# Optimization experiments

Hardware: AMD Instinct MI355X
Metric: run time of the kernel (lower is better)

The kernel has to match this reference:

```python
import jax, jax.numpy as jnp
import numpy as np

G = 56          # voxel grid resolution per axis
N = 65536
K = 27          # 3x3x3 kernel offsets
C_IN = 128
C_OUT = 128


def _build_rulebook():
    """Submanifold conv rulebook: for each kernel offset, (input_row, output_row) pairs.

    Padded to P=N pairs per offset; invalid pairs use in_idx=0 and out_idx=N
    (a dummy output slot that is dropped), so shapes are static.
    """
    rng = np.random.default_rng(0)
    keys = np.sort(rng.choice(G ** 3, size=N, replace=False)).astype(np.int64)
    x = keys // (G * G)
    y = (keys // G) % G
    z = keys % G
    in_idx = np.zeros((K, N), dtype=np.int32)
    out_idx = np.full((K, N), N, dtype=np.int32)
    k = 0
    for dx in (-1, 0, 1):
        for dy in (-1, 0, 1):
            for dz in (-1, 0, 1):
                nx, ny, nz = x + dx, y + dy, z + dz
                valid = (nx >= 0) & (nx < G) & (ny >= 0) & (ny < G) & (nz >= 0) & (nz < G)
                nkey = (nx * G + ny) * G + nz
                pos = np.searchsorted(keys, np.clip(nkey, 0, G ** 3 - 1))
                pos = np.clip(pos, 0, N - 1)
                found = valid & (keys[pos] == nkey)
                cnt = int(found.sum())
                in_idx[k, :cnt] = pos[found]
                out_idx[k, :cnt] = np.nonzero(found)[0]
                k += 1
    return jnp.asarray(in_idx), jnp.asarray(out_idx)


def setup_inputs() -> dict:
    key = jax.random.key(0)
    k1, k2, k3 = jax.random.split(key, 3)
    fan_in = K * C_IN
    features = jax.random.normal(k1, (N, C_IN), dtype=jnp.float32)
    weight = jax.random.normal(k2, (K, C_IN, C_OUT), dtype=jnp.float32) * (1.0 / np.sqrt(fan_in))
    bias = jax.random.normal(k3, (C_OUT,), dtype=jnp.float32) * 0.01
    in_idx, out_idx = _build_rulebook()
    return {"features": features, "weight": weight, "bias": bias,
            "in_idx": in_idx, "out_idx": out_idx}


def reference(features, weight, bias, in_idx, out_idx):
    # gather: [K, P, C_in]
    gathered = features[in_idx]
    # per-offset GEMM: [K, P, C_out]
    contrib = jnp.einsum('kpc,kcd->kpd', gathered, weight)
    n = features.shape[0]
    c_out = weight.shape[-1]
    # scatter-accumulate into N real rows + 1 dummy row for padded pairs
    out = jnp.zeros((n + 1, c_out), dtype=features.dtype)
    out = out.at[out_idx.reshape(-1)].add(contrib.reshape(-1, c_out))
    return out[:n] + bias
```

## Files before the change

### kernel.cpp

```cpp
#include <hip/hip_runtime.h>
#include <hip/hip_bf16.h>
#include <stdint.h>

#define NV   65536
#define KOFF 27
#define CIN  128
#define COUT 128

typedef __bf16 bf16x8 __attribute__((ext_vector_type(8)));
typedef float  f32x16 __attribute__((ext_vector_type(16)));

__device__ __forceinline__ void async_copy16(void* lds, const void* g) {
    __builtin_amdgcn_global_load_lds(
        (const __attribute__((address_space(1))) void*)g,
        (__attribute__((address_space(3))) void*)lds,
        16, 0, 0);
}

#define JOB_A_BLOCKS 4097
#define JOB_B_BLOCKS 108
#define JOB_S_BLOCKS 1728

__global__ void k_prep_all(const float* __restrict__ f,
                           uint4* __restrict__ fb4,
                           const float* __restrict__ w,
                           __hip_bfloat16* __restrict__ wt,
                           const int4* __restrict__ in4,
                           const int4* __restrict__ out4,
                           int* __restrict__ nbr) {
    __shared__ float tb[64][65];
    const int b = blockIdx.x;
    const int t = threadIdx.x;
    if (b < JOB_A_BLOCKS) {
        int i = b * 256 + t;
        int total8  = (NV + 1) * CIN / 8;
        int nvalid8 = NV * CIN / 8;
        if (i >= total8) return;
        union { uint4 u; __hip_bfloat16 h[8]; } p;
        if (i < nvalid8) {
            const float4* f4 = (const float4*)f;
            float4 a = f4[i * 2];
            float4 c = f4[i * 2 + 1];
            p.h[0] = __float2bfloat16(a.x);
            p.h[1] = __float2bfloat16(a.y);
            p.h[2] = __float2bfloat16(a.z);
            p.h[3] = __float2bfloat16(a.w);
            p.h[4] = __float2bfloat16(c.x);
            p.h[5] = __float2bfloat16(c.y);
            p.h[6] = __float2bfloat16(c.z);
            p.h[7] = __float2bfloat16(c.w);
        } else {
            p.u = make_uint4(0, 0, 0, 0);
        }
        fb4[i] = p.u;
    } else if (b < JOB_A_BLOCKS + JOB_B_BLOCKS) {
        int bb = b - JOB_A_BLOCKS;
        int k    = bb >> 2;
        int r0   = ((bb >> 1) & 1) * 64;
        int c0   = (bb & 1) * 64;
        const float* wk = w + k * 16384;
        __hip_bfloat16* wtk = wt + k * 16384;
        #pragma unroll
        for (int j = 0; j < 16; ++j) {
            int lrow = j * 4 + (t >> 6);
            int lcol = t & 63;
            tb[lrow][lcol] = wk[(r0 + lrow) * 128 + (c0 + lcol)];
        }
        __syncthreads();
        #pragma unroll
        for (int j = 0; j < 16; ++j) {
            int orow = j * 4 + (t >> 6);
            int ocol = t & 63;
            wtk[(c0 + orow) * 128 + (r0 + ocol)] = __float2bfloat16(tb[ocol][orow]);
        }
    } else {
        int i = (b - JOB_A_BLOCKS - JOB_B_BLOCKS) * 256 + t;
        int k = i >> 14;
        int4 ii = in4[i];
        int4 oo = out4[i];
        int* nb = nbr + k * (NV + 1);
        nb[oo.x] = ii.x;
        nb[oo.y] = ii.y;
        nb[oo.z] = ii.z;
        nb[oo.w] = ii.w;
    }
}

__global__ __launch_bounds__(256, 2)
void sp_conv_main(const __hip_bfloat16* __restrict__ feats,
                  const __hip_bfloat16* __restrict__ wt,
                  const int* __restrict__ nbr,
                  const float* __restrict__ bias,
                  float* __restrict__ out) {
    __shared__ unsigned char smem[65536];
    unsigned char* smA = smem;
    unsigned char* smB = smem + 32768;

    const int t   = threadIdx.x;
    const int bid = blockIdx.x;
    const int tile0 = ((bid & 7) * 64 + (bid >> 3)) * 128;

    const int w    = t >> 6;
    const int lane = t & 63;
    const int l31  = lane & 31;
    const int half = lane >> 5;
    const int m0   = (w >> 1) * 64;
    const int n0   = (w & 1) * 64;

    const int srow   = t >> 4;
    const int sbyte  = ((t & 15) ^ srow) * 16;

    f32x16 acc[2][2] = {};

    const unsigned char* featsB = (const unsigned char*)feats;
    const unsigned char* wtB    = (const unsigned char*)wt;

    int arows[8];
    {
        const int* nbr0 = nbr + tile0;
        #pragma unroll
        for (int i = 0; i < 8; ++i) arows[i] = nbr0[i * 16 + srow];
    }

    for (int k = 0; k < KOFF; ++k) {
        const unsigned char* wk = wtB + (size_t)k * 32768;
        #pragma unroll
        for (int i = 0; i < 8; ++i) {
            unsigned ar = min((unsigned)arows[i], (unsigned)NV);
            async_copy16(smA + i * 4096 + t * 16,
                         featsB + (size_t)ar * 256 + sbyte);
            async_copy16(smB + i * 4096 + t * 16,
                         wk + (i * 16 + srow) * 256 + sbyte);
        }
        __syncthreads();

        if (k + 1 < KOFF) {
            const int* nbrn = nbr + (k + 1) * (NV + 1) + tile0;
            #pragma unroll
            for (int i = 0; i < 8; ++i) arows[i] = nbrn[i * 16 + srow];
        }

        #pragma unroll
        for (int ks = 0; ks < 8; ++ks) {
            const int c = ks * 2 + half;
            bf16x8 af[2], bfr[2];
            #pragma unroll
            for (int mt = 0; mt < 2; ++mt) {
                int row = m0 + mt * 32 + l31;
                af[mt] = *(const bf16x8*)(smA + row * 256 + ((c ^ (row & 15)) * 16));
            }
            #pragma unroll
            for (int nt = 0; nt < 2; ++nt) {
                int row = n0 + nt * 32 + l31;
                bfr[nt] = *(const bf16x8*)(smB + row * 256 + ((c ^ (row & 15)) * 16));
            }
            #pragma unroll
            for (int mt = 0; mt < 2; ++mt)
                #pragma unroll
                for (int nt = 0; nt < 2; ++nt)
                    acc[mt][nt] = __builtin_amdgcn_mfma_f32_32x32x16_bf16(
                        af[mt], bfr[nt], acc[mt][nt], 0, 0, 0);
        }
        __syncthreads();
    }

    float bv[2];
    #pragma unroll
    for (int nt = 0; nt < 2; ++nt) bv[nt] = bias[n0 + nt * 32 + l31];

    #pragma unroll
    for (int mt = 0; mt < 2; ++mt) {
        #pragma unroll
        for (int nt = 0; nt < 2; ++nt) {
            #pragma unroll
            for (int r = 0; r < 16; ++r) {
                int rrow = (r & 3) + 8 * (r >> 2) + 4 * half;
                int grow = tile0 + m0 + mt * 32 + rrow;
                out[(size_t)grow * COUT + n0 + nt * 32 + l31] =
                    acc[mt][nt][r] + bv[nt];
            }
        }
    }
}


extern "C" void kernel_launch(void* const* d_in, const int* in_sizes, int n_in,
                              void* d_out, int out_size, void* d_ws, size_t ws_size,
                              hipStream_t stream) {
    const float* features = (const float*)d_in[0];
    const float* weight   = (const float*)d_in[1];
    const float* bias     = (const float*)d_in[2];
    const int*   in_idx   = (const int*)d_in[3];
    const int*   out_idx  = (const int*)d_in[4];
    float* out = (float*)d_out;

    uint8_t* ws = (uint8_t*)d_ws;
    size_t off = 0;
    __hip_bfloat16* feats_bf = (__hip_bfloat16*)(ws + off);
    off += (size_t)(NV + 1) * CIN * 2;
    off = (off + 255) & ~(size_t)255;
    __hip_bfloat16* wt_bf = (__hip_bfloat16*)(ws + off);
    off += (size_t)KOFF * CIN * COUT * 2;
    off = (off + 255) & ~(size_t)255;
    int* nbr = (int*)(ws + off);

    hipMemsetAsync(nbr, 0xFF, (size_t)KOFF * (NV + 1) * 4, stream);

    k_prep_all<<<JOB_A_BLOCKS + JOB_B_BLOCKS + JOB_S_BLOCKS, 256, 0, stream>>>(
        features, (uint4*)feats_bf, weight, wt_bf,
        (const int4*)in_idx, (const int4*)out_idx, nbr);

    sp_conv_main<<<NV / 128, 256, 0, stream>>>(feats_bf, wt_bf, nbr, bias, out);
}
```

Baseline: 167.2 us.

## Prepack weights into MFMA fragments in registers and double-buffer gathered features

Weights are now pre-packed into per-lane MFMA B fragments during prep and loaded straight into registers, so they no longer pass through LDS. The gathered feature tile is double-buffered in LDS: the next offset's rows are prefetched asynchronously while the current offset is computed, and each iteration needs one barrier instead of two. The warp split changes to 128x32 per wave using 16x16x32 MFMA, so each wave reuses the full A tile against its own weight columns. This costs more registers (32 accumulator vectors plus two sets of B fragments), which may hurt occupancy under launch_bounds(256,2).

```diff
diff --git a/kernel.cpp b/kernel.cpp
--- a/kernel.cpp
+++ b/kernel.cpp
@@ -8,7 +8,7 @@
 #define COUT 128
 
 typedef __bf16 bf16x8 __attribute__((ext_vector_type(8)));
-typedef float  f32x16 __attribute__((ext_vector_type(16)));
+typedef float  f32x4  __attribute__((ext_vector_type(4)));
 
 __device__ __forceinline__ void async_copy16(void* lds, const void* g) {
     __builtin_amdgcn_global_load_lds(
@@ -18,17 +18,16 @@
 }
 
 #define JOB_A_BLOCKS 4097
-#define JOB_B_BLOCKS 108
+#define JOB_B_BLOCKS 216
 #define JOB_S_BLOCKS 1728
 
 __global__ void k_prep_all(const float* __restrict__ f,
                            uint4* __restrict__ fb4,
                            const float* __restrict__ w,
-                           __hip_bfloat16* __restrict__ wt,
+                           uint4* __restrict__ wfrag4,
                            const int4* __restrict__ in4,
                            const int4* __restrict__ out4,
                            int* __restrict__ nbr) {
-    __shared__ float tb[64][65];
     const int b = blockIdx.x;
     const int t = threadIdx.x;
     if (b < JOB_A_BLOCKS) {
@@ -54,25 +53,20 @@
         }
         fb4[i] = p.u;
     } else if (b < JOB_A_BLOCKS + JOB_B_BLOCKS) {
-        int bb = b - JOB_A_BLOCKS;
-        int k    = bb >> 2;
-        int r0   = ((bb >> 1) & 1) * 64;
-        int c0   = (bb & 1) * 64;
+        int c    = (b - JOB_A_BLOCKS) * 256 + t;
+        int lane = c & 63;
+        int nt   = (c >> 6) & 1;
+        int ks   = (c >> 7) & 3;
+        int wv   = (c >> 9) & 3;
+        int k    = c >> 11;
+        int cout = wv * 32 + nt * 16 + (lane & 15);
+        int cin0 = ks * 32 + (lane >> 4) * 8;
         const float* wk = w + k * 16384;
-        __hip_bfloat16* wtk = wt + k * 16384;
-        #pragma unroll
-        for (int j = 0; j < 16; ++j) {
-            int lrow = j * 4 + (t >> 6);
-            int lcol = t & 63;
-            tb[lrow][lcol] = wk[(r0 + lrow) * 128 + (c0 + lcol)];
-        }
-        __syncthreads();
-        #pragma unroll
-        for (int j = 0; j < 16; ++j) {
-            int orow = j * 4 + (t >> 6);
-            int ocol = t & 63;
-            wtk[(c0 + orow) * 128 + (r0 + ocol)] = __float2bfloat16(tb[ocol][orow]);
-        }
+        union { uint4 u; __hip_bfloat16 h[8]; } p;
+        #pragma unroll
+        for (int j = 0; j < 8; ++j)
+            p.h[j] = __float2bfloat16(wk[(cin0 + j) * 128 + cout]);
+        wfrag4[c] = p.u;
     } else {
         int i = (b - JOB_A_BLOCKS - JOB_B_BLOCKS) * 256 + t;
         int k = i >> 14;
@@ -88,13 +82,11 @@
 
 __global__ __launch_bounds__(256, 2)
 void sp_conv_main(const __hip_bfloat16* __restrict__ feats,
-                  const __hip_bfloat16* __restrict__ wt,
+                  const uint4* __restrict__ wfrag,
                   const int* __restrict__ nbr,
                   const float* __restrict__ bias,
                   float* __restrict__ out) {
     __shared__ unsigned char smem[65536];
-    unsigned char* smA = smem;
-    unsigned char* smB = smem + 32768;
 
     const int t   = threadIdx.x;
     const int bid = blockIdx.x;
@@ -102,18 +94,15 @@
 
     const int w    = t >> 6;
     const int lane = t & 63;
-    const int l31  = lane & 31;
-    const int half = lane >> 5;
-    const int m0   = (w >> 1) * 64;
-    const int n0   = (w & 1) * 64;
+    const int lr   = lane & 15;
+    const int quad = lane >> 4;
 
     const int srow   = t >> 4;
     const int sbyte  = ((t & 15) ^ srow) * 16;
 
-    f32x16 acc[2][2] = {};
+    f32x4 acc[8][2] = {};
 
     const unsigned char* featsB = (const unsigned char*)feats;
-    const unsigned char* wtB    = (const unsigned char*)wt;
 
     int arows[8];
     {
@@ -121,62 +110,91 @@
         #pragma unroll
         for (int i = 0; i < 8; ++i) arows[i] = nbr0[i * 16 + srow];
     }
-
+    #pragma unroll
+    for (int i = 0; i < 8; ++i) {
+        unsigned ar = min((unsigned)arows[i], (unsigned)NV);
+        async_copy16(smem + i * 4096 + t * 16,
+                     featsB + (size_t)ar * 256 + sbyte);
+    }
+    {
+        const int* nbr1 = nbr + (NV + 1) + tile0;
+        #pragma unroll
+        for (int i = 0; i < 8; ++i) arows[i] = nbr1[i * 16 + srow];
+    }
+    uint4 bcur[4][2], bnext[4][2];
+    {
+        const uint4* wf0 = wfrag + w * 512 + lane;
+        #pragma unroll
+        for (int ks = 0; ks < 4; ++ks)
+            #pragma unroll
+            for (int nt = 0; nt < 2; ++nt)
+                bcur[ks][nt] = wf0[ks * 128 + nt * 64];
+    }
+    __syncthreads();
+
+    int cbuf = 0;
     for (int k = 0; k < KOFF; ++k) {
-        const unsigned char* wk = wtB + (size_t)k * 32768;
-        #pragma unroll
-        for (int i = 0; i < 8; ++i) {
-            unsigned ar = min((unsigned)arows[i], (unsigned)NV);
-            async_copy16(smA + i * 4096 + t * 16,
-                         featsB + (size_t)ar * 256 + sbyte);
-            async_copy16(smB + i * 4096 + t * 16,
-                         wk + (i * 16 + srow) * 256 + sbyte);
-        }
-        __syncthreads();
-
         if (k + 1 < KOFF) {
-            const int* nbrn = nbr + (k + 1) * (NV + 1) + tile0;
-            #pragma unroll
-            for (int i = 0; i < 8; ++i) arows[i] = nbrn[i * 16 + srow];
-        }
-
-        #pragma unroll
-        for (int ks = 0; ks < 8; ++ks) {
-            const int c = ks * 2 + half;
-            bf16x8 af[2], bfr[2];
-            #pragma unroll
-            for (int mt = 0; mt < 2; ++mt) {
-                int row = m0 + mt * 32 + l31;
-                af[mt] = *(const bf16x8*)(smA + row * 256 + ((c ^ (row & 15)) * 16));
-            }
-            #pragma unroll
-            for (int nt = 0; nt < 2; ++nt) {
-                int row = n0 + nt * 32 + l31;
-                bfr[nt] = *(const bf16x8*)(smB + row * 256 + ((c ^ (row & 15)) * 16));
-            }
-            #pragma unroll
-            for (int mt = 0; mt < 2; ++mt)
+            unsigned char* dst = smem + (cbuf ^ 1) * 32768;
+            #pragma unroll
+            for (int i = 0; i < 8; ++i) {
+                unsigned ar = min((unsigned)arows[i], (unsigned)NV);
+                async_copy16(dst + i * 4096 + t * 16,
+                             featsB + (size_t)ar * 256 + sbyte);
+            }
+            if (k + 2 < KOFF) {
+                const int* nbrn = nbr + (k + 2) * (NV + 1) + tile0;
+                #pragma unroll
+                for (int i = 0; i < 8; ++i) arows[i] = nbrn[i * 16 + srow];
+            }
+            const uint4* wfn = wfrag + (k + 1) * 2048 + w * 512 + lane;
+            #pragma unroll
+            for (int ks = 0; ks < 4; ++ks)
                 #pragma unroll
                 for (int nt = 0; nt < 2; ++nt)
-                    acc[mt][nt] = __builtin_amdgcn_mfma_f32_32x32x16_bf16(
-                        af[mt], bfr[nt], acc[mt][nt], 0, 0, 0);
+                    bnext[ks][nt] = wfn[ks * 128 + nt * 64];
+        }
+
+        const unsigned char* base = smem + cbuf * 32768;
+        #pragma unroll
+        for (int ks = 0; ks < 4; ++ks) {
+            bf16x8 af[8];
+            #pragma unroll
+            for (int mt = 0; mt < 8; ++mt) {
+                int row = mt * 16 + lr;
+                af[mt] = *(const bf16x8*)(base + row * 256 +
+                                          (((ks * 4 + quad) ^ lr) * 16));
+            }
+            #pragma unroll
+            for (int mt = 0; mt < 8; ++mt)
+                #pragma unroll
+                for (int nt = 0; nt < 2; ++nt)
+                    acc[mt][nt] = __builtin_amdgcn_mfma_f32_16x16x32_bf16(
+                        af[mt], *(const bf16x8*)&bcur[ks][nt],
+                        acc[mt][nt], 0, 0, 0);
         }
         __syncthreads();
-    }
-
+        #pragma unroll
+        for (int ks = 0; ks < 4; ++ks)
+            #pragma unroll
+            for (int nt = 0; nt < 2; ++nt)
+                bcur[ks][nt] = bnext[ks][nt];
+        cbuf ^= 1;
+    }
+
+    const int n0w = w * 32;
     float bv[2];
     #pragma unroll
-    for (int nt = 0; nt < 2; ++nt) bv[nt] = bias[n0 + nt * 32 + l31];
+    for (int nt = 0; nt < 2; ++nt) bv[nt] = bias[n0w + nt * 16 + lr];
 
     #pragma unroll
-    for (int mt = 0; mt < 2; ++mt) {
+    for (int mt = 0; mt < 8; ++mt) {
         #pragma unroll
         for (int nt = 0; nt < 2; ++nt) {
             #pragma unroll
-            for (int r = 0; r < 16; ++r) {
-                int rrow = (r & 3) + 8 * (r >> 2) + 4 * half;
-                int grow = tile0 + m0 + mt * 32 + rrow;
-                out[(size_t)grow * COUT + n0 + nt * 32 + l31] =
+            for (int r = 0; r < 4; ++r) {
+                int grow = tile0 + mt * 16 + quad * 4 + r;
+                out[(size_t)grow * COUT + n0w + nt * 16 + lr] =
                     acc[mt][nt][r] + bv[nt];
             }
         }
@@ -199,7 +217,7 @@
     __hip_bfloat16* feats_bf = (__hip_bfloat16*)(ws + off);
     off += (size_t)(NV + 1) * CIN * 2;
     off = (off + 255) & ~(size_t)255;
-    __hip_bfloat16* wt_bf = (__hip_bfloat16*)(ws + off);
+    uint4* wfrag = (uint4*)(ws + off);
     off += (size_t)KOFF * CIN * COUT * 2;
     off = (off + 255) & ~(size_t)255;
     int* nbr = (int*)(ws + off);
@@ -207,8 +225,8 @@
     hipMemsetAsync(nbr, 0xFF, (size_t)KOFF * (NV + 1) * 4, stream);
 
     k_prep_all<<<JOB_A_BLOCKS + JOB_B_BLOCKS + JOB_S_BLOCKS, 256, 0, stream>>>(
-        features, (uint4*)feats_bf, weight, wt_bf,
+        features, (uint4*)feats_bf, weight, wfrag,
         (const int4*)in_idx, (const int4*)out_idx, nbr);
 
-    sp_conv_main<<<NV / 128, 256, 0, stream>>>(feats_bf, wt_bf, nbr, bias, out);
-}
+    sp_conv_main<<<NV / 128, 256, 0, stream>>>(feats_bf, wfrag, nbr, bias, out);
+}
```

Result: faster. 158.2 us (-5.4%).
